# Kernel optimization log

Measured on AMD Instinct MI355X. Metric: run time of the kernel, lower is better.

Reference implementation:

```python
import jax, jax.numpy as jnp
import numpy as np


def lstm_cell(x, h, c, Wi, Wh, b):
    # PyTorch LSTMCell gate order: i, f, g, o
    g = x @ Wi.T + h @ Wh.T + b
    i, f, gg, o = jnp.split(g, 4, axis=-1)
    c = jax.nn.sigmoid(f) * c + jax.nn.sigmoid(i) * jnp.tanh(gg)
    h = jax.nn.sigmoid(o) * jnp.tanh(c)
    return h, c


def setup_inputs() -> dict:
    key = jax.random.key(0)
    ks = jax.random.split(key, 32)
    S, B, L, N, T = 20, 16, 30, 6, 20
    H, E, Vs, Vt = 512, 512, 50000, 30000
    w = lambda k, shape: jax.random.normal(k, shape, jnp.float32) * 0.05
    return {
        'articles': jax.random.randint(ks[0], (S, B, L), 0, Vs, jnp.int32),
        'summaries': jax.random.randint(ks[1], (N, B, T), 0, Vt, jnp.int32),
        'emb_src': w(ks[2], (Vs, E)),
        'emb_tgt': w(ks[3], (Vt, E)),
        'we_Wi': w(ks[4], (4 * H, E)), 'we_Wh': w(ks[5], (4 * H, H)), 'we_b': w(ks[6], (4 * H,)),
        'se_Wi': w(ks[7], (4 * H, H)), 'se_Wh': w(ks[8], (4 * H, H)), 'se_b': w(ks[9], (4 * H,)),
        'W_feat': w(ks[10], (H, H)), 'b_feat': w(ks[11], (H,)),
        'wd_Wi': w(ks[12], (4 * H, E)), 'wd_Wh': w(ks[13], (4 * H, H)), 'wd_b': w(ks[14], (4 * H,)),
        'W_vocab': w(ks[15], (Vt, H)), 'b_vocab': w(ks[16], (Vt,)),
        'sd_Wi': w(ks[17], (4 * H, H)), 'sd_Wh': w(ks[18], (4 * H, H)), 'sd_b': w(ks[19], (4 * H,)),
        'attn_Wh': w(ks[20], (H, H)), 'attn_wc': w(ks[21], (H,)), 'attn_v': w(ks[22], (H,)),
        'W_out': w(ks[23], (H, 2 * H)), 'b_out': w(ks[24], (H,)),
    }


def _forward(articles, summaries, emb_src, emb_tgt, we_Wi, we_Wh, we_b,
             se_Wi, se_Wh, se_b, W_feat, b_feat, wd_Wi, wd_Wh, wd_b,
             W_vocab, b_vocab, sd_Wi, sd_Wh, sd_b, attn_Wh, attn_wc, attn_v,
             W_out, b_out):
    S, B, L = articles.shape
    H = we_Wh.shape[1]

    # ---- word encoder: LSTMCell over each sentence, vmapped over S ----
    def encode_sentence(tokens):  # [B, L]
        x = emb_src[tokens]  # [B, L, E]
        z = jnp.zeros((B, H), x.dtype)
        def step(hc, xt):
            h, c = lstm_cell(xt, hc[0], hc[1], we_Wi, we_Wh, we_b)
            return (h, c), None
        (h, _), _ = jax.lax.scan(step, (z, z), jnp.swapaxes(x, 0, 1))
        return h
    word_hx = jax.vmap(encode_sentence)(articles)  # [S, B, H]

    # ---- sentence encoder: LSTM over sentence dim ----
    z = jnp.zeros((B, H), word_hx.dtype)
    def senc_step(hc, x):
        h, c = lstm_cell(x, hc[0], hc[1], se_Wi, se_Wh, se_b)
        return (h, c), h
    (s_hx, s_cx), sent_out = jax.lax.scan(senc_step, (z, z), word_hx)  # sent_out [S,B,H]
    sent_feat = sent_out @ W_feat.T + b_feat  # precomputed attention features

    mask = (articles[:, :, 0:1] > 0).astype(jnp.float32)  # [S, B, 1]
    coverage0 = jnp.zeros_like(mask)

    # ---- hierarchical decoder over summary sentences ----
    def sent_step(carry, sent):  # sent [B, T]
        w_hx, w_cx, s_hx, s_cx, coverage, loss = carry
        seq = sent.T  # [T, B]

        def word_step(wc, ba):
            wh, wcell, l = wc
            wb, wa = ba
            wh, wcell = lstm_cell(emb_tgt[wb], wh, wcell, wd_Wi, wd_Wh, wd_b)
            logits = wh @ W_vocab.T + b_vocab  # [B, V]
            logp = jax.nn.log_softmax(logits, axis=-1)
            nll = -jnp.take_along_axis(logp, wa[:, None], axis=1)[:, 0]
            m = (wa != 0).astype(logits.dtype)  # ignore_index=0
            l = l + jnp.sum(nll * m) / jnp.maximum(jnp.sum(m), 1.0)
            return (wh, wcell, l), None

        (w_hx, w_cx, loss), _ = jax.lax.scan(word_step, (w_hx, w_cx, loss), (seq[:-1], seq[1:]))

        # sentence decoder step with coverage attention over S sentences
        s_h2, s_cx = lstm_cell(w_hx, s_hx, s_cx, sd_Wi, sd_Wh, sd_b)
        e = jnp.einsum('sbh,h->sb', jnp.tanh(sent_feat + s_h2 @ attn_Wh.T + coverage * attn_wc), attn_v)
        e = jnp.where(mask[:, :, 0] > 0, e, -1e9)
        align = jax.nn.softmax(e, axis=0)[:, :, None]  # [S, B, 1]
        context = jnp.sum(align * sent_out, axis=0)  # [B, H]
        final = jnp.tanh(jnp.concatenate([context, s_h2], axis=-1) @ W_out.T + b_out)
        # coverage loss (with pre-update coverage), then accumulate coverage
        loss = loss + jnp.mean(jnp.sum(jnp.minimum(align[:, :, 0], coverage[:, :, 0]), axis=0))
        coverage = coverage + align
        return (final, w_cx, final, s_cx, coverage, loss), None

    init = (s_hx, s_cx, s_hx, s_cx, coverage0, jnp.float32(0.0))
    (_, _, _, _, _, loss), _ = jax.lax.scan(sent_step, init, summaries)
    return loss


def reference(articles, summaries, emb_src, emb_tgt, we_Wi, we_Wh, we_b,
              se_Wi, se_Wh, se_b, W_feat, b_feat, wd_Wi, wd_Wh, wd_b,
              W_vocab, b_vocab, sd_Wi, sd_Wh, sd_b, attn_Wh, attn_wc, attn_v,
              W_out, b_out):
    return _forward(articles, summaries, emb_src, emb_tgt, we_Wi, we_Wh, we_b,
                    se_Wi, se_Wh, se_b, W_feat, b_feat, wd_Wi, wd_Wh, wd_b,
                    W_vocab, b_vocab, sd_Wi, sd_Wh, sd_b, attn_Wh, attn_wc,
                    attn_v, W_out, b_out)
```

## Files before the change

### kernel.cpp

```cpp
#include <hip/hip_runtime.h>
#include <cstdint>
#include <cstddef>

#define H 512
#define SS 20
#define BB 16
#define LL 30
#define NN 6
#define TT 20
#define VT 30000
#define MROWS 1824
#define NSTEPS 114
#define MPAD 1856
#define NT2 120
#define UBLK 16
#define NV 232
#define MEGA 248

#define SCOPE_AGENT __HIP_MEMORY_SCOPE_AGENT

typedef __attribute__((ext_vector_type(8))) short bf16x8;
typedef __attribute__((ext_vector_type(4))) float f32x4;

__device__ __forceinline__ float sigmoidf_(float x) { return 1.f / (1.f + expf(-x)); }
__device__ __forceinline__ float b2f(ushort u) { return __uint_as_float(((uint32_t)u) << 16); }
__device__ __forceinline__ ushort f2b_rne(float f) {
  uint32_t u = __float_as_uint(f);
  return (ushort)((u + 0x7fffu + ((u >> 16) & 1u)) >> 16);
}

__device__ __forceinline__ void ast_u32(uint* p, uint v) {
  __hip_atomic_store(p, v, __ATOMIC_RELAXED, SCOPE_AGENT);
}
__device__ __forceinline__ uint ald_u32(const uint* p) {
  return __hip_atomic_load(p, __ATOMIC_RELAXED, SCOPE_AGENT);
}

__device__ __forceinline__ void sbar(uint* flags, int slot, int nblk, uint phase)
{
  __syncthreads();
  if (threadIdx.x == 0) {
    __builtin_amdgcn_fence(__ATOMIC_RELEASE, "agent");
    ast_u32(&flags[slot * 16], phase);
  }
  if ((int)threadIdx.x < nblk) {
    while (ald_u32(&flags[threadIdx.x * 16]) < phase)
      __builtin_amdgcn_s_sleep(1);
  }
  __syncthreads();
  if (threadIdx.x == 0)
    __builtin_amdgcn_fence(__ATOMIC_ACQUIRE, "agent");
  __syncthreads();
}

struct PrepP {
  const int* articles; const int* summaries;
  const float* emb_src; const float* emb_tgt;
  const float* we_Wi; const float* wd_Wi; const float* we_Wh;
  const float* se_Wi; const float* se_Wh; const float* W_feat;
  const float* wd_Wh; const float* sd_Wi; const float* sd_Wh;
  const float* attn_Wh; const float* W_out;
  ushort* A_we; ushort* A_wd;
  ushort* weWi; ushort* wdWi; ushort* weWh;
  ushort* seWi; ushort* seWh; ushort* wfeat;
  ushort* wdWh; ushort* sdWi; ushort* sdWh;
  ushort* attnWh; ushort* Wout;
};

__device__ __forceinline__ void conv_f2b(const float* __restrict__ src,
                                         ushort* __restrict__ dst, int n4,
                                         int t0, int stride)
{
  for (int i = t0; i < n4; i += stride) {
    float4 v = reinterpret_cast<const float4*>(src)[i];
    ushort4 o;
    o.x = f2b_rne(v.x); o.y = f2b_rne(v.y);
    o.z = f2b_rne(v.z); o.w = f2b_rne(v.w);
    reinterpret_cast<ushort4*>(dst)[i] = o;
  }
}

__global__ __launch_bounds__(256) void prep_kernel(PrepP P)
{
  const int t0 = blockIdx.x * 256 + threadIdx.x;
  const int stride = gridDim.x * 256;
  for (int i = t0; i < SS * BB * LL * H; i += stride) {
    int m = i >> 9, k = i & 511;
    int l = m / (SS * BB), sb = m % (SS * BB);
    int tok = P.articles[sb * LL + l];
    P.A_we[i] = f2b_rne(P.emb_src[(size_t)tok * H + k]);
  }
  for (int i = t0; i < MROWS * H; i += stride) {
    int m = i >> 9, k = i & 511;
    int stp = m >> 4, b = m & 15;
    int n = stp / (TT - 1), t = stp % (TT - 1);
    int tok = P.summaries[(n * BB + b) * TT + t];
    P.A_wd[i] = f2b_rne(P.emb_tgt[(size_t)tok * H + k]);
  }
  const int Q = 4 * H * H / 4;
  conv_f2b(P.we_Wi, P.weWi, Q, t0, stride);
  conv_f2b(P.wd_Wi, P.wdWi, Q, t0, stride);
  conv_f2b(P.we_Wh, P.weWh, Q, t0, stride);
  conv_f2b(P.se_Wi, P.seWi, Q, t0, stride);
  conv_f2b(P.se_Wh, P.seWh, Q, t0, stride);
  conv_f2b(P.wd_Wh, P.wdWh, Q, t0, stride);
  conv_f2b(P.sd_Wi, P.sdWi, Q, t0, stride);
  conv_f2b(P.sd_Wh, P.sdWh, Q, t0, stride);
  conv_f2b(P.W_feat, P.wfeat, H * H / 4, t0, stride);
  conv_f2b(P.attn_Wh, P.attnWh, H * H / 4, t0, stride);
  conv_f2b(P.W_out, P.Wout, H * 2 * H / 4, t0, stride);
}

__global__ __launch_bounds__(512) void proj_mfma_kernel(
    const ushort* __restrict__ A_we, const ushort* __restrict__ weWi,
    const float* __restrict__ we_b, ushort* __restrict__ XiW,
    const ushort* __restrict__ A_wd, const ushort* __restrict__ wdWi,
    const float* __restrict__ wd_b, ushort* __restrict__ XiD)
{
  int bid = blockIdx.x;
  const ushort* A; const ushort* W; const float* bias; ushort* C; int M, mt, nt;
  if (bid < 1200) { A = A_we; W = weWi; bias = we_b; C = XiW; M = 9600; mt = bid >> 3; nt = bid & 7; }
  else { int b2 = bid - 1200; A = A_wd; W = wdWi; bias = wd_b; C = XiD; M = MROWS; mt = b2 >> 3; nt = b2 & 7; }
  const int tid = threadIdx.x, wid = tid >> 6, lane = tid & 63;
  const int wm = wid >> 2, wn = wid & 3;
  const int m0 = mt * 64 + wm * 32, n0 = nt * 256 + wn * 64;
  const int lr = lane & 15, lk = (lane >> 4) << 3;

  f32x4 acc[2][4];
#pragma unroll
  for (int i = 0; i < 2; ++i)
#pragma unroll
    for (int nf = 0; nf < 4; ++nf) acc[i][nf] = (f32x4)0.0f;

  for (int k0 = 0; k0 < H; k0 += 32) {
    bf16x8 a[2], b[4];
#pragma unroll
    for (int i = 0; i < 2; ++i) {
      int m = m0 + i * 16 + lr;
      bf16x8 az = (bf16x8)(short)0;
      if (m < M) az = *reinterpret_cast<const bf16x8*>(A + (size_t)m * H + k0 + lk);
      a[i] = az;
    }
#pragma unroll
    for (int nf = 0; nf < 4; ++nf)
      b[nf] = *reinterpret_cast<const bf16x8*>(W + (size_t)(n0 + nf * 16 + lr) * H + k0 + lk);
#pragma unroll
    for (int i = 0; i < 2; ++i)
#pragma unroll
      for (int nf = 0; nf < 4; ++nf)
        acc[i][nf] = __builtin_amdgcn_mfma_f32_16x16x32_bf16(a[i], b[nf], acc[i][nf], 0, 0, 0);
  }
#pragma unroll
  for (int i = 0; i < 2; ++i)
#pragma unroll
    for (int nf = 0; nf < 4; ++nf) {
      int n = n0 + nf * 16 + lr;
      float bv = bias[n];
#pragma unroll
      for (int jreg = 0; jreg < 4; ++jreg) {
        int row = m0 + i * 16 + (lane >> 4) * 4 + jreg;
        if (row < M) C[(size_t)row * 2048 + n] = f2b_rne(acc[i][nf][jreg] + bv);
      }
    }
}

struct MP {
  const ushort* XiW; const ushort* XiD;
  const ushort* weWh; const ushort* seWi; const ushort* seWh;
  const ushort* wfeat; const ushort* wdWh; const ushort* sdWi;
  const ushort* sdWh; const ushort* attnWh; const ushort* Wout;
  const float* se_b; const float* b_feat; const float* sd_b; const float* b_out;
  const float* attn_wc; const float* attn_v; const int* articles;
  ushort* h0; ushort* h1;
  float* XiS;
  ushort* sh0; ushort* sh1;
  float* sent_out; ushort* sent_out_bf; float* sent_feat;
  ushort* wh_bf; ushort* sdh_bf; ushort* final_bf; ushort* catb;
  float* qb; float* ebuf; float* alignb; float* covb; float* loss;
  uint* sflags;
  uint* vbflags;
  uint* vflag;
  const float* Wv; ushort* Wv_bf; const float* bv; float* partials;
};

__global__ __launch_bounds__(512) void mega_kernel(MP P)
{
  const int tid = threadIdx.x, bid = blockIdx.x;
  const int wid = tid >> 6, lane = tid & 63;
  const int lr = lane & 15;
  const int lk = (lane >> 4) << 3;
  const int orow = (lane >> 4) << 2;

  if (bid >= UBLK) {
    const int v = bid - UBLK;
    const int mt = v >> 3, chunk = v & 7;
    __shared__ float red[4][64][2];

    if (tid == 0) {
      while (ald_u32(P.vflag) < 1u) __builtin_amdgcn_s_sleep(16);
    }
    __syncthreads();
    {
      const int n4 = VT * H / 4;
      for (int i = v * 512 + tid; i < n4; i += NV * 512) {
        float4 w = reinterpret_cast<const float4*>(P.Wv)[i];
        ushort4 o;
        o.x = f2b_rne(w.x); o.y = f2b_rne(w.y);
        o.z = f2b_rne(w.z); o.w = f2b_rne(w.w);
        reinterpret_cast<ushort4*>(P.Wv_bf)[i] = o;
      }
    }
    sbar(P.vbflags, v, NV, 1u);

    {
      int lastStep = mt * 4 + 3; if (lastStep > 113) lastStep = 113;
      uint want = 2u + (uint)(lastStep / 19);
      if (tid == 0) {
        while (ald_u32(P.vflag) < want) __builtin_amdgcn_s_sleep(16);
        __builtin_amdgcn_fence(__ATOMIC_ACQUIRE, "agent");
      }
      __syncthreads();
    }

    const int wm = wid >> 2, wn = wid & 3;
    const int m0 = mt * 64 + wm * 32;
    bf16x8 areg[2][16];
#pragma unroll
    for (int i = 0; i < 2; ++i)
#pragma unroll
      for (int kk = 0; kk < 16; ++kk)
        areg[i][kk] = *reinterpret_cast<const bf16x8*>(
            P.wh_bf + (size_t)(m0 + i * 16 + lr) * H + kk * 32 + lk);

    for (int nt2 = 0; nt2 < 15; ++nt2) {
      const int n0 = chunk * 3840 + nt2 * 256 + wn * 64;
      f32x4 acc[2][4];
#pragma unroll
      for (int i = 0; i < 2; ++i)
#pragma unroll
        for (int nf = 0; nf < 4; ++nf) acc[i][nf] = (f32x4)0.0f;

#pragma unroll 4
      for (int kk = 0; kk < 16; ++kk) {
        bf16x8 b[4];
#pragma unroll
        for (int nf = 0; nf < 4; ++nf) {
          int n = n0 + nf * 16 + lr;
          bf16x8 bz = (bf16x8)(short)0;
          if (n < VT) bz = *reinterpret_cast<const bf16x8*>(P.Wv_bf + (size_t)n * H + kk * 32 + lk);
          b[nf] = bz;
        }
#pragma unroll
        for (int i = 0; i < 2; ++i)
#pragma unroll
          for (int nf = 0; nf < 4; ++nf)
            acc[i][nf] = __builtin_amdgcn_mfma_f32_16x16x32_bf16(areg[i][kk], b[nf], acc[i][nf], 0, 0, 0);
      }

      float bc[4];
      int val[4];
#pragma unroll
      for (int nf = 0; nf < 4; ++nf) {
        int n = n0 + nf * 16 + lr;
        val[nf] = (n < VT);
        bc[nf] = val[nf] ? P.bv[n] : 0.f;
      }
#pragma unroll
      for (int i = 0; i < 2; ++i) {
#pragma unroll
        for (int jreg = 0; jreg < 4; ++jreg) {
          float lg[4];
          float mx = -3.0e38f;
#pragma unroll
          for (int nf = 0; nf < 4; ++nf) {
            lg[nf] = val[nf] ? (acc[i][nf][jreg] + bc[nf]) : -3.0e38f;
            mx = fmaxf(mx, lg[nf]);
          }
#pragma unroll
          for (int d = 1; d < 16; d <<= 1) mx = fmaxf(mx, __shfl_xor(mx, d));
          float s = 0.f;
#pragma unroll
          for (int nf = 0; nf < 4; ++nf) s += val[nf] ? expf(lg[nf] - mx) : 0.f;
#pragma unroll
          for (int d = 1; d < 16; d <<= 1) s += __shfl_xor(s, d);
          if (lr == 0) {
            int rloc = wm * 32 + i * 16 + (lane >> 4) * 4 + jreg;
            red[wn][rloc][0] = mx;
            red[wn][rloc][1] = s;
          }
        }
      }
      __syncthreads();
      if (tid < 64) {
        int r2 = tid;
        float M = -3.0e38f;
#pragma unroll
        for (int w = 0; w < 4; ++w) M = fmaxf(M, red[w][r2][0]);
        float S = 0.f;
#pragma unroll
        for (int w = 0; w < 4; ++w) S += red[w][r2][1] * expf(red[w][r2][0] - M);
        size_t p = ((size_t)(mt * 64 + r2) * NT2 + chunk * 15 + nt2) * 2;
        P.partials[p] = M;
        P.partials[p + 1] = S;
      }
      __syncthreads();
    }
    return;
  }

  __shared__ f32x4 hred[2][4][64];
  const int gw = bid * 8 + wid;
  uint ph = 0;

  {
    float cst[5][4];
#pragma unroll
    for (int it = 0; it < 5; ++it)
#pragma unroll
      for (int rg = 0; rg < 4; ++rg) cst[it][rg] = 0.f;
    ushort* cur = P.h0;
    ushort* nxt = P.h1;
    const int ug = gw & 31;
    const int unit = ug * 16 + lr;
    const ushort* wb = P.weWh + (size_t)(ug * 16 + lr) * H + lk;
    for (int l = 0; l < LL; ++l) {
#pragma unroll
      for (int it = 0; it < 5; ++it) {
        int mt = (gw + it * 128) >> 5;
        f32x4 acc[4];
#pragma unroll
        for (int g = 0; g < 4; ++g) acc[g] = (f32x4)0.0f;
        const ushort* ab = cur + (size_t)(mt * 16 + lr) * H + lk;
#pragma unroll
        for (int k0 = 0; k0 < H; k0 += 32) {
          bf16x8 a = *reinterpret_cast<const bf16x8*>(ab + k0);
#pragma unroll
          for (int g = 0; g < 4; ++g) {
            bf16x8 b = *reinterpret_cast<const bf16x8*>(wb + (size_t)g * H * H + k0);
            acc[g] = __builtin_amdgcn_mfma_f32_16x16x32_bf16(a, b, acc[g], 0, 0, 0);
          }
        }
#pragma unroll
        for (int rg = 0; rg < 4; ++rg) {
          int row = mt * 16 + orow + rg;
          const ushort* xi = P.XiW + (size_t)(l * 320 + row) * 2048 + unit;
          float gi = acc[0][rg] + b2f(xi[0]);
          float gf = acc[1][rg] + b2f(xi[512]);
          float gc = acc[2][rg] + b2f(xi[1024]);
          float go = acc[3][rg] + b2f(xi[1536]);
          float c = sigmoidf_(gf) * cst[it][rg] + sigmoidf_(gi) * tanhf(gc);
          float h = sigmoidf_(go) * tanhf(c);
          cst[it][rg] = c;
          nxt[(size_t)row * H + unit] = f2b_rne(h);
        }
      }
      sbar(P.sflags, bid, UBLK, ++ph);
      ushort* t = cur; cur = nxt; nxt = t;
    }
    {
      const ushort* wbs = P.seWi + (size_t)(ug * 16 + lr) * H + lk;
#pragma unroll
      for (int it = 0; it < 5; ++it) {
        int mt = (gw + it * 128) >> 5;
        f32x4 acc[4];
#pragma unroll
        for (int g = 0; g < 4; ++g) acc[g] = (f32x4)0.0f;
        const ushort* ab = cur + (size_t)(mt * 16 + lr) * H + lk;
#pragma unroll
        for (int k0 = 0; k0 < H; k0 += 32) {
          bf16x8 a = *reinterpret_cast<const bf16x8*>(ab + k0);
#pragma unroll
          for (int g = 0; g < 4; ++g) {
            bf16x8 b = *reinterpret_cast<const bf16x8*>(wbs + (size_t)g * H * H + k0);
            acc[g] = __builtin_amdgcn_mfma_f32_16x16x32_bf16(a, b, acc[g], 0, 0, 0);
          }
        }
#pragma unroll
        for (int rg = 0; rg < 4; ++rg) {
          int row = mt * 16 + orow + rg;
#pragma unroll
          for (int g = 0; g < 4; ++g)
            P.XiS[(size_t)row * 2048 + g * H + unit] = acc[g][rg] + P.se_b[g * H + unit];
        }
      }
    }
    sbar(P.sflags, bid, UBLK, ++ph);
    if (bid == 0 && tid == 0)
      __hip_atomic_store(P.vflag, 1u, __ATOMIC_RELEASE, SCOPE_AGENT);
  }

  float cw[4] = {0.f, 0.f, 0.f, 0.f};
  float csd[4] = {0.f, 0.f, 0.f, 0.f};
  {
    float cse[4] = {0.f, 0.f, 0.f, 0.f};
    ushort* cur = P.sh0;
    ushort* nxt = P.sh1;
    const int ug = bid * 2 + wid;
    const int unit = ug * 16 + lr;
    for (int s = 0; s < SS; ++s) {
      if (wid < 2) {
        f32x4 acc[4];
#pragma unroll
        for (int g = 0; g < 4; ++g) acc[g] = (f32x4)0.0f;
        const ushort* ab = cur + (size_t)lr * H + lk;
        const ushort* wb = P.seWh + (size_t)(ug * 16 + lr) * H + lk;
#pragma unroll
        for (int k0 = 0; k0 < H; k0 += 32) {
          bf16x8 a = *reinterpret_cast<const bf16x8*>(ab + k0);
#pragma unroll
          for (int g = 0; g < 4; ++g) {
            bf16x8 b = *reinterpret_cast<const bf16x8*>(wb + (size_t)g * H * H + k0);
            acc[g] = __builtin_amdgcn_mfma_f32_16x16x32_bf16(a, b, acc[g], 0, 0, 0);
          }
        }
#pragma unroll
        for (int rg = 0; rg < 4; ++rg) {
          int row = orow + rg;
          const float* xi = P.XiS + (size_t)(s * 16 + row) * 2048 + unit;
          float gi = acc[0][rg] + xi[0];
          float gf = acc[1][rg] + xi[512];
          float gc = acc[2][rg] + xi[1024];
          float go = acc[3][rg] + xi[1536];
          float c = sigmoidf_(gf) * cse[rg] + sigmoidf_(gi) * tanhf(gc);
          float h = sigmoidf_(go) * tanhf(c);
          cse[rg] = c;
          nxt[(size_t)row * H + unit] = f2b_rne(h);
          P.sent_out[(size_t)(s * 16 + row) * H + unit] = h;
          P.sent_out_bf[(size_t)(s * 16 + row) * H + unit] = f2b_rne(h);
        }
      }
      sbar(P.sflags, bid, UBLK, ++ph);
      ushort* t = cur; cur = nxt; nxt = t;
    }
    if (wid < 2) {
      f32x4 v; v[0] = cse[0]; v[1] = cse[1]; v[2] = cse[2]; v[3] = cse[3];
      hred[wid][0][lane] = v;
#pragma unroll
      for (int rg = 0; rg < 4; ++rg) csd[rg] = cse[rg];
    }
    __syncthreads();
    if (wid < 4 && !(wid & 1)) {
      f32x4 v = hred[wid >> 1][0][lane];
      cw[0] = v[0]; cw[1] = v[1]; cw[2] = v[2]; cw[3] = v[3];
    }
    __syncthreads();
  }

  {
    const int ug = gw & 31;
    const int unit = ug * 16 + lr;
    const ushort* wb = P.wfeat + (size_t)(ug * 16 + lr) * H + lk;
#pragma unroll
    for (int it = 0; it < 5; ++it) {
      int mt = (gw + it * 128) >> 5;
      f32x4 acc = (f32x4)0.0f;
      const ushort* ab = P.sent_out_bf + (size_t)(mt * 16 + lr) * H + lk;
#pragma unroll
      for (int k0 = 0; k0 < H; k0 += 32) {
        bf16x8 a = *reinterpret_cast<const bf16x8*>(ab + k0);
        bf16x8 b = *reinterpret_cast<const bf16x8*>(wb + k0);
        acc = __builtin_amdgcn_mfma_f32_16x16x32_bf16(a, b, acc, 0, 0, 0);
      }
#pragma unroll
      for (int rg = 0; rg < 4; ++rg) {
        int row = mt * 16 + orow + rg;
        P.sent_feat[(size_t)row * H + unit] = acc[rg] + P.b_feat[unit];
      }
    }
    sbar(P.sflags, bid, UBLK, ++ph);
  }

  {
    const int half = wid & 1;
    const int ug2 = bid * 2 + (wid >> 1);
    const int unit2 = ug2 * 16 + lr;
    const int ug = bid * 2 + wid;
    const int unit = ug * 16 + lr;

    for (int n = 0; n < NN; ++n) {
      bf16x8 wreg[4][8];
      if (wid < 4) {
#pragma unroll
        for (int g = 0; g < 4; ++g)
#pragma unroll
          for (int kk = 0; kk < 8; ++kk)
            wreg[g][kk] = *reinterpret_cast<const bf16x8*>(
                P.wdWh + (size_t)g * H * H + (size_t)(ug2 * 16 + lr) * H +
                half * 256 + kk * 32 + lk);
      }
      for (int t = 0; t < TT - 1; ++t) {
        int stp = n * (TT - 1) + t;
        f32x4 acc[4];
        if (wid < 4) {
          const ushort* A = (t == 0)
              ? ((n == 0) ? P.sh0 : P.final_bf)
              : P.wh_bf + (size_t)(stp - 1) * 16 * H;
#pragma unroll
          for (int g = 0; g < 4; ++g) acc[g] = (f32x4)0.0f;
          const ushort* ab = A + (size_t)lr * H + half * 256 + lk;
#pragma unroll
          for (int kk = 0; kk < 8; ++kk) {
            bf16x8 a = *reinterpret_cast<const bf16x8*>(ab + kk * 32);
#pragma unroll
            for (int g = 0; g < 4; ++g)
              acc[g] = __builtin_amdgcn_mfma_f32_16x16x32_bf16(a, wreg[g][kk], acc[g], 0, 0, 0);
          }
          if (half) {
#pragma unroll
            for (int g = 0; g < 4; ++g) hred[wid >> 1][g][lane] = acc[g];
          }
        }
        __syncthreads();
        if (wid < 4 && !half) {
#pragma unroll
          for (int g = 0; g < 4; ++g) acc[g] += hred[wid >> 1][g][lane];
#pragma unroll
          for (int rg = 0; rg < 4; ++rg) {
            int row = orow + rg;
            const ushort* xi = P.XiD + (size_t)(stp * 16 + row) * 2048 + unit2;
            float gi = acc[0][rg] + b2f(xi[0]);
            float gf = acc[1][rg] + b2f(xi[512]);
            float gc = acc[2][rg] + b2f(xi[1024]);
            float go = acc[3][rg] + b2f(xi[1536]);
            float c = sigmoidf_(gf) * cw[rg] + sigmoidf_(gi) * tanhf(gc);
            float h = sigmoidf_(go) * tanhf(c);
            cw[rg] = c;
            P.wh_bf[(size_t)(stp * 16 + row) * H + unit2] = f2b_rne(h);
          }
        }
        sbar(P.sflags, bid, UBLK, ++ph);
      }
      if (bid == 0 && tid == 0)
        __hip_atomic_store(P.vflag, 2u + (uint)n, __ATOMIC_RELEASE, SCOPE_AGENT);
      if (wid < 2) {
        f32x4 acc[4];
#pragma unroll
        for (int g = 0; g < 4; ++g) acc[g] = (f32x4)0.0f;
        const ushort* A1 = P.wh_bf + (size_t)(n * (TT - 1) + TT - 2) * 16 * H;
        const ushort* A2 = (n == 0) ? P.sh0 : P.final_bf;
        const ushort* ab1 = A1 + (size_t)lr * H + lk;
        const ushort* wb1 = P.sdWi + (size_t)(ug * 16 + lr) * H + lk;
#pragma unroll
        for (int k0 = 0; k0 < H; k0 += 32) {
          bf16x8 a = *reinterpret_cast<const bf16x8*>(ab1 + k0);
#pragma unroll
          for (int g = 0; g < 4; ++g) {
            bf16x8 b = *reinterpret_cast<const bf16x8*>(wb1 + (size_t)g * H * H + k0);
            acc[g] = __builtin_amdgcn_mfma_f32_16x16x32_bf16(a, b, acc[g], 0, 0, 0);
          }
        }
        const ushort* ab2 = A2 + (size_t)lr * H + lk;
        const ushort* wb2 = P.sdWh + (size_t)(ug * 16 + lr) * H + lk;
#pragma unroll
        for (int k0 = 0; k0 < H; k0 += 32) {
          bf16x8 a = *reinterpret_cast<const bf16x8*>(ab2 + k0);
#pragma unroll
          for (int g = 0; g < 4; ++g) {
            bf16x8 b = *reinterpret_cast<const bf16x8*>(wb2 + (size_t)g * H * H + k0);
            acc[g] = __builtin_amdgcn_mfma_f32_16x16x32_bf16(a, b, acc[g], 0, 0, 0);
          }
        }
#pragma unroll
        for (int rg = 0; rg < 4; ++rg) {
          int row = orow + rg;
          float gi = acc[0][rg] + P.sd_b[0 * H + unit];
          float gf = acc[1][rg] + P.sd_b[1 * H + unit];
          float gc = acc[2][rg] + P.sd_b[2 * H + unit];
          float go = acc[3][rg] + P.sd_b[3 * H + unit];
          float c = sigmoidf_(gf) * csd[rg] + sigmoidf_(gi) * tanhf(gc);
          float h = sigmoidf_(go) * tanhf(c);
          csd[rg] = c;
          P.sdh_bf[(size_t)row * H + unit] = f2b_rne(h);
        }
      }
      sbar(P.sflags, bid, UBLK, ++ph);
      if (wid < 2) {
        f32x4 acc = (f32x4)0.0f;
        const ushort* ab = P.sdh_bf + (size_t)lr * H + lk;
        const ushort* wb = P.attnWh + (size_t)(ug * 16 + lr) * H + lk;
#pragma unroll
        for (int k0 = 0; k0 < H; k0 += 32) {
          bf16x8 a = *reinterpret_cast<const bf16x8*>(ab + k0);
          bf16x8 b = *reinterpret_cast<const bf16x8*>(wb + k0);
          acc = __builtin_amdgcn_mfma_f32_16x16x32_bf16(a, b, acc, 0, 0, 0);
        }
#pragma unroll
        for (int rg = 0; rg < 4; ++rg)
          P.qb[(size_t)(orow + rg) * H + unit] = acc[rg];
      }
      sbar(P.sflags, bid, UBLK, ++ph);
      for (int sb = gw; sb < 320; sb += 128) {
        int b = sb & 15;
        float cov = P.covb[sb];
        float sum = 0.f;
        for (int h2 = lane; h2 < H; h2 += 64)
          sum += tanhf(P.sent_feat[(size_t)sb * H + h2] + P.qb[b * H + h2] +
                       cov * P.attn_wc[h2]) * P.attn_v[h2];
#pragma unroll
        for (int d = 1; d < 64; d <<= 1) sum += __shfl_xor(sum, d);
        if (lane == 0)
          P.ebuf[sb] = (P.articles[sb * LL] > 0) ? sum : -1e9f;
      }
      sbar(P.sflags, bid, UBLK, ++ph);
      if (wid == 0) {
        int b = bid;
        float ev = (lane < SS) ? P.ebuf[lane * 16 + b] : -3.0e38f;
        float mx = ev;
#pragma unroll
        for (int d = 1; d < 64; d <<= 1) mx = fmaxf(mx, __shfl_xor(mx, d));
        float ex = (lane < SS) ? expf(ev - mx) : 0.f;
        float s = ex;
#pragma unroll
        for (int d = 1; d < 64; d <<= 1) s += __shfl_xor(s, d);
        float al = ex / s;
        float cl = 0.f;
        if (lane < SS) {
          int sb = lane * 16 + b;
          float cov = P.covb[sb];
          cl = fminf(al, cov);
          P.covb[sb] = cov + al;
          P.alignb[sb] = al;
        }
#pragma unroll
        for (int d = 1; d < 64; d <<= 1) cl += __shfl_xor(cl, d);
        if (lane == 0) atomicAdd(P.loss, cl * (1.f / BB));
      }
      __syncthreads();
      {
        int b = bid, h2 = tid;
        float s = 0.f;
#pragma unroll
        for (int ss2 = 0; ss2 < SS; ++ss2)
          s += P.alignb[ss2 * 16 + b] * P.sent_out[(size_t)(ss2 * 16 + b) * H + h2];
        P.catb[b * 1024 + h2] = f2b_rne(s);
        P.catb[b * 1024 + 512 + h2] = P.sdh_bf[(size_t)b * H + h2];
      }
      sbar(P.sflags, bid, UBLK, ++ph);
      if (wid < 2) {
        f32x4 acc = (f32x4)0.0f;
        const ushort* ab = P.catb + (size_t)lr * 1024 + lk;
        const ushort* wb = P.Wout + (size_t)(ug * 16 + lr) * 1024 + lk;
#pragma unroll
        for (int k0 = 0; k0 < 1024; k0 += 32) {
          bf16x8 a = *reinterpret_cast<const bf16x8*>(ab + k0);
          bf16x8 b = *reinterpret_cast<const bf16x8*>(wb + k0);
          acc = __builtin_amdgcn_mfma_f32_16x16x32_bf16(a, b, acc, 0, 0, 0);
        }
#pragma unroll
        for (int rg = 0; rg < 4; ++rg) {
          int row = orow + rg;
          float v = tanhf(acc[rg] + P.b_out[unit]);
          P.final_bf[(size_t)row * H + unit] = f2b_rne(v);
        }
      }
      sbar(P.sflags, bid, UBLK, ++ph);
    }
    if (bid == 0 && tid == 0)
      __hip_atomic_store(P.vflag, 7u, __ATOMIC_RELEASE, SCOPE_AGENT);
  }
}

__global__ void tlog_kernel(const ushort* __restrict__ wh_bf,
                            const ushort* __restrict__ Wv_bf,
                            const float* __restrict__ bv,
                            const int* __restrict__ summaries,
                            float* __restrict__ tlog)
{
  int row = blockIdx.x;
  int lane = threadIdx.x;
  int b = row & 15, stp = row >> 4;
  int n = stp / (TT - 1), t = stp % (TT - 1);
  int tgt = summaries[(n * BB + b) * TT + t + 1];
  float s = 0.f;
  for (int k = lane; k < H; k += 64)
    s += b2f(wh_bf[(size_t)row * H + k]) * b2f(Wv_bf[(size_t)tgt * H + k]);
#pragma unroll
  for (int d = 1; d < 64; d <<= 1) s += __shfl_xor(s, d);
  if (lane == 0) tlog[row] = s + bv[tgt];
}

__global__ __launch_bounds__(256) void nll_kernel(
    const float* __restrict__ partials, const float* __restrict__ tlog,
    const int* __restrict__ summaries, float* __restrict__ loss)
{
  int stp = blockIdx.x;
  int tid = threadIdx.x;
  int rr = tid >> 4, ch = tid & 15;
  int row = stp * 16 + rr;
  const float* pr = partials + (size_t)row * NT2 * 2;
  float mx = -3.0e38f;
  for (int t2 = ch; t2 < NT2; t2 += 16) mx = fmaxf(mx, pr[t2 * 2]);
#pragma unroll
  for (int d = 1; d < 16; d <<= 1) mx = fmaxf(mx, __shfl_xor(mx, d));
  float s = 0.f;
  for (int t2 = ch; t2 < NT2; t2 += 16) s += pr[t2 * 2 + 1] * expf(pr[t2 * 2] - mx);
#pragma unroll
  for (int d = 1; d < 16; d <<= 1) s += __shfl_xor(s, d);
  __shared__ float sh_n[16], sh_m[16];
  if (ch == 0) {
    float lse = mx + logf(s);
    float nll = lse - tlog[row];
    int b = row & 15;
    int n = stp / (TT - 1), t = stp % (TT - 1);
    int wa = summaries[(n * BB + b) * TT + t + 1];
    sh_n[rr] = (wa != 0) ? nll : 0.f;
    sh_m[rr] = (wa != 0) ? 1.f : 0.f;
  }
  __syncthreads();
  if (tid == 0) {
    float sn = 0.f, sm = 0.f;
    for (int r2 = 0; r2 < 16; ++r2) { sn += sh_n[r2]; sm += sh_m[r2]; }
    atomicAdd(loss, sn / fmaxf(sm, 1.f));
  }
}

extern "C" void kernel_launch(void* const* d_in, const int* in_sizes, int n_in,
                              void* d_out, int out_size, void* d_ws, size_t ws_size,
                              hipStream_t stream)
{
  (void)in_sizes; (void)n_in; (void)out_size; (void)ws_size;
  const int*   articles  = (const int*)d_in[0];
  const int*   summaries = (const int*)d_in[1];
  const float* emb_src   = (const float*)d_in[2];
  const float* emb_tgt   = (const float*)d_in[3];
  const float* we_Wi = (const float*)d_in[4];
  const float* we_Wh = (const float*)d_in[5];
  const float* we_b  = (const float*)d_in[6];
  const float* se_Wi = (const float*)d_in[7];
  const float* se_Wh = (const float*)d_in[8];
  const float* se_b  = (const float*)d_in[9];
  const float* W_feat = (const float*)d_in[10];
  const float* b_feat = (const float*)d_in[11];
  const float* wd_Wi = (const float*)d_in[12];
  const float* wd_Wh = (const float*)d_in[13];
  const float* wd_b  = (const float*)d_in[14];
  const float* W_vocab = (const float*)d_in[15];
  const float* b_vocab = (const float*)d_in[16];
  const float* sd_Wi = (const float*)d_in[17];
  const float* sd_Wh = (const float*)d_in[18];
  const float* sd_b  = (const float*)d_in[19];
  const float* attn_Wh = (const float*)d_in[20];
  const float* attn_wc = (const float*)d_in[21];
  const float* attn_v  = (const float*)d_in[22];
  const float* W_out = (const float*)d_in[23];
  const float* b_out = (const float*)d_in[24];

  char* wsb = (char*)d_ws;
  size_t off = 0;
  auto alloc = [&](size_t bytes) -> char* {
    char* p = wsb + off;
    off += (bytes + 255) & ~(size_t)255;
    return p;
  };

  char* regA = alloc(9830400);
  ushort* A_we     = (ushort*)regA;
  ushort* wh_bf    = (ushort*)regA;
  float*  partials = (float*)(regA + 1900544);
  float*  tlogb    = (float*)(regA + 3682304);

  ushort* A_wd = (ushort*)alloc((size_t)MROWS * H * 2);

  char* regW = alloc((size_t)9600 * 2048 * 2);
  ushort* XiW   = (ushort*)regW;
  ushort* Wv_bf = (ushort*)regW;

  ushort* XiD = (ushort*)alloc((size_t)MROWS * 2048 * 2);

  ushort* weWi  = (ushort*)alloc(4 * H * H * 2);
  ushort* wdWi  = (ushort*)alloc(4 * H * H * 2);
  ushort* weWh  = (ushort*)alloc(4 * H * H * 2);
  ushort* seWi  = (ushort*)alloc(4 * H * H * 2);
  ushort* seWh  = (ushort*)alloc(4 * H * H * 2);
  ushort* wdWh  = (ushort*)alloc(4 * H * H * 2);
  ushort* sdWi  = (ushort*)alloc(4 * H * H * 2);
  ushort* sdWh  = (ushort*)alloc(4 * H * H * 2);
  ushort* wfeat = (ushort*)alloc(H * H * 2);
  ushort* attnWh= (ushort*)alloc(H * H * 2);
  ushort* Wout  = (ushort*)alloc(H * 2 * H * 2);

  float*  XiS = (float*)alloc((size_t)320 * 2048 * 4);
  ushort* h0  = (ushort*)alloc(320 * H * 2);
  ushort* h1  = (ushort*)alloc(320 * H * 2);
  ushort* sh0 = (ushort*)alloc(16 * H * 2);
  ushort* sh1 = (ushort*)alloc(16 * H * 2);
  float*  sent_out    = (float*)alloc(320 * H * 4);
  ushort* sent_out_bf = (ushort*)alloc(320 * H * 2);
  float*  sent_feat   = (float*)alloc(320 * H * 4);
  ushort* sdh_bf   = (ushort*)alloc(16 * H * 2);
  ushort* final_bf = (ushort*)alloc(16 * H * 2);
  ushort* catb     = (ushort*)alloc(16 * 1024 * 2);
  float*  qb       = (float*)alloc(16 * H * 4);
  float*  ebuf   = (float*)alloc(1280);
  float*  alignb = (float*)alloc(1280);
  float*  covb   = (float*)alloc(1280);
  uint*   sflags  = (uint*)alloc(UBLK * 16 * 4);
  uint*   vbflags = (uint*)alloc(NV * 16 * 4);
  uint*   vflag   = (uint*)alloc(256);

  float* loss = (float*)d_out;
  hipMemsetAsync(loss, 0, 4, stream);
  hipMemsetAsync(covb, 0, 1280, stream);
  hipMemsetAsync(h0, 0, 320 * H * 2, stream);
  hipMemsetAsync(sh0, 0, 16 * H * 2, stream);
  hipMemsetAsync(sflags, 0, UBLK * 16 * 4, stream);
  hipMemsetAsync(vbflags, 0, NV * 16 * 4, stream);
  hipMemsetAsync(vflag, 0, 256, stream);

  {
    PrepP P = {articles, summaries, emb_src, emb_tgt,
               we_Wi, wd_Wi, we_Wh, se_Wi, se_Wh, W_feat,
               wd_Wh, sd_Wi, sd_Wh, attn_Wh, W_out,
               A_we, A_wd, weWi, wdWi, weWh, seWi, seWh, wfeat,
               wdWh, sdWi, sdWh, attnWh, Wout};
    prep_kernel<<<2048, 256, 0, stream>>>(P);
  }

  proj_mfma_kernel<<<1432, 512, 0, stream>>>(A_we, weWi, we_b, XiW,
                                             A_wd, wdWi, wd_b, XiD);

  hipMemsetAsync((char*)wh_bf + (size_t)MROWS * H * 2, 0,
                 (size_t)(MPAD - MROWS) * H * 2, stream);

  {
    MP P;
    P.XiW = XiW; P.XiD = XiD;
    P.weWh = weWh; P.seWi = seWi; P.seWh = seWh; P.wfeat = wfeat;
    P.wdWh = wdWh; P.sdWi = sdWi; P.sdWh = sdWh; P.attnWh = attnWh; P.Wout = Wout;
    P.se_b = se_b; P.b_feat = b_feat; P.sd_b = sd_b; P.b_out = b_out;
    P.attn_wc = attn_wc; P.attn_v = attn_v; P.articles = articles;
    P.h0 = h0; P.h1 = h1; P.XiS = XiS; P.sh0 = sh0; P.sh1 = sh1;
    P.sent_out = sent_out; P.sent_out_bf = sent_out_bf; P.sent_feat = sent_feat;
    P.wh_bf = wh_bf; P.sdh_bf = sdh_bf; P.final_bf = final_bf; P.catb = catb;
    P.qb = qb; P.ebuf = ebuf; P.alignb = alignb; P.covb = covb; P.loss = loss;
    P.sflags = sflags; P.vbflags = vbflags; P.vflag = vflag;
    P.Wv = W_vocab; P.Wv_bf = Wv_bf; P.bv = b_vocab; P.partials = partials;
    mega_kernel<<<MEGA, 512, 0, stream>>>(P);
  }

  tlog_kernel<<<MROWS, 64, 0, stream>>>(wh_bf, Wv_bf, b_vocab, summaries, tlogb);
  nll_kernel<<<NSTEPS, 256, 0, stream>>>(partials, tlogb, summaries, loss);
}
```

Before: 5.032 ms.

## Spread sequential blocks across XCDs and keep attention state per block in LDS

The 16 sequential recurrence blocks now use block ids that are multiples of 8 below 128, so they land on different XCDs instead of packing onto one. The vocab-worker blocks are renumbered to fill the remaining ids. Each sequential block owns one batch element, so the attention energies, alignment and coverage now live in shared memory. This drops one grid-wide barrier per decoder step along with the global ebuf, alignb and covb buffers. The risks are more L2 traffic across XCDs for shared recurrent state, and each block now computes all 20 energies for its batch element, which adds some per-block work.

```diff
diff --git a/kernel.cpp b/kernel.cpp
--- a/kernel.cpp
+++ b/kernel.cpp
@@ -176,7 +176,7 @@
   ushort* sh0; ushort* sh1;
   float* sent_out; ushort* sent_out_bf; float* sent_feat;
   ushort* wh_bf; ushort* sdh_bf; ushort* final_bf; ushort* catb;
-  float* qb; float* ebuf; float* alignb; float* covb; float* loss;
+  float* qb; float* loss;
   uint* sflags;
   uint* vbflags;
   uint* vflag;
@@ -191,8 +191,10 @@
   const int lk = (lane >> 4) << 3;
   const int orow = (lane >> 4) << 2;
 
-  if (bid >= UBLK) {
-    const int v = bid - UBLK;
+  const bool isSeq = (bid < 128) && ((bid & 7) == 0);
+
+  if (!isSeq) {
+    const int v = (bid < 128) ? (bid - (bid >> 3) - 1) : (bid - UBLK);
     const int mt = v >> 3, chunk = v & 7;
     __shared__ float red[4][64][2];
 
@@ -213,8 +215,8 @@
     sbar(P.vbflags, v, NV, 1u);
 
     {
-      int lastStep = mt * 4 + 3; if (lastStep > 113) lastStep = 113;
-      uint want = 2u + (uint)(lastStep / 19);
+      int lastStep = mt * 4 + 3; if (lastStep > NSTEPS - 1) lastStep = NSTEPS - 1;
+      uint want = 2u + (uint)(lastStep / (TT - 1));
       if (tid == 0) {
         while (ald_u32(P.vflag) < want) __builtin_amdgcn_s_sleep(16);
         __builtin_amdgcn_fence(__ATOMIC_ACQUIRE, "agent");
@@ -295,10 +297,10 @@
         int r2 = tid;
         float M = -3.0e38f;
 #pragma unroll
-        for (int w = 0; w < 4; ++w) M = fmaxf(M, red[w][r2][0]);
+        for (int q = 0; q < 4; ++q) M = fmaxf(M, red[q][r2][0]);
         float S = 0.f;
 #pragma unroll
-        for (int w = 0; w < 4; ++w) S += red[w][r2][1] * expf(red[w][r2][0] - M);
+        for (int q = 0; q < 4; ++q) S += red[q][r2][1] * expf(red[q][r2][0] - M);
         size_t p = ((size_t)(mt * 64 + r2) * NT2 + chunk * 15 + nt2) * 2;
         P.partials[p] = M;
         P.partials[p + 1] = S;
@@ -308,8 +310,10 @@
     return;
   }
 
+  const int sid = bid >> 3;
   __shared__ f32x4 hred[2][4][64];
-  const int gw = bid * 8 + wid;
+  __shared__ float e_l[SS], align_l[SS], cov_l[SS];
+  const int gw = sid * 8 + wid;
   uint ph = 0;
 
   {
@@ -354,7 +358,7 @@
           nxt[(size_t)row * H + unit] = f2b_rne(h);
         }
       }
-      sbar(P.sflags, bid, UBLK, ++ph);
+      sbar(P.sflags, sid, UBLK, ++ph);
       ushort* t = cur; cur = nxt; nxt = t;
     }
     {
@@ -384,8 +388,8 @@
         }
       }
     }
-    sbar(P.sflags, bid, UBLK, ++ph);
-    if (bid == 0 && tid == 0)
+    sbar(P.sflags, sid, UBLK, ++ph);
+    if (sid == 0 && tid == 0)
       __hip_atomic_store(P.vflag, 1u, __ATOMIC_RELEASE, SCOPE_AGENT);
   }
 
@@ -395,7 +399,7 @@
     float cse[4] = {0.f, 0.f, 0.f, 0.f};
     ushort* cur = P.sh0;
     ushort* nxt = P.sh1;
-    const int ug = bid * 2 + wid;
+    const int ug = sid * 2 + wid;
     const int unit = ug * 16 + lr;
     for (int s = 0; s < SS; ++s) {
       if (wid < 2) {
@@ -429,7 +433,7 @@
           P.sent_out_bf[(size_t)(s * 16 + row) * H + unit] = f2b_rne(h);
         }
       }
-      sbar(P.sflags, bid, UBLK, ++ph);
+      sbar(P.sflags, sid, UBLK, ++ph);
       ushort* t = cur; cur = nxt; nxt = t;
     }
     if (wid < 2) {
@@ -467,15 +471,17 @@
         P.sent_feat[(size_t)row * H + unit] = acc[rg] + P.b_feat[unit];
       }
     }
-    sbar(P.sflags, bid, UBLK, ++ph);
+    if (tid < SS) cov_l[tid] = 0.f;
+    sbar(P.sflags, sid, UBLK, ++ph);
   }
 
   {
     const int half = wid & 1;
-    const int ug2 = bid * 2 + (wid >> 1);
+    const int ug2 = sid * 2 + (wid >> 1);
     const int unit2 = ug2 * 16 + lr;
-    const int ug = bid * 2 + wid;
+    const int ug = sid * 2 + wid;
     const int unit = ug * 16 + lr;
+    const int b_ = sid;
 
     for (int n = 0; n < NN; ++n) {
       bf16x8 wreg[4][8];
@@ -528,9 +534,9 @@
             P.wh_bf[(size_t)(stp * 16 + row) * H + unit2] = f2b_rne(h);
           }
         }
-        sbar(P.sflags, bid, UBLK, ++ph);
-      }
-      if (bid == 0 && tid == 0)
+        sbar(P.sflags, sid, UBLK, ++ph);
+      }
+      if (sid == 0 && tid == 0)
         __hip_atomic_store(P.vflag, 2u + (uint)n, __ATOMIC_RELEASE, SCOPE_AGENT);
       if (wid < 2) {
         f32x4 acc[4];
@@ -573,7 +579,7 @@
           P.sdh_bf[(size_t)row * H + unit] = f2b_rne(h);
         }
       }
-      sbar(P.sflags, bid, UBLK, ++ph);
+      sbar(P.sflags, sid, UBLK, ++ph);
       if (wid < 2) {
         f32x4 acc = (f32x4)0.0f;
         const ushort* ab = P.sdh_bf + (size_t)lr * H + lk;
@@ -588,23 +594,21 @@
         for (int rg = 0; rg < 4; ++rg)
           P.qb[(size_t)(orow + rg) * H + unit] = acc[rg];
       }
-      sbar(P.sflags, bid, UBLK, ++ph);
-      for (int sb = gw; sb < 320; sb += 128) {
-        int b = sb & 15;
-        float cov = P.covb[sb];
+      sbar(P.sflags, sid, UBLK, ++ph);
+      for (int s = wid; s < SS; s += 8) {
+        float cov = cov_l[s];
         float sum = 0.f;
         for (int h2 = lane; h2 < H; h2 += 64)
-          sum += tanhf(P.sent_feat[(size_t)sb * H + h2] + P.qb[b * H + h2] +
-                       cov * P.attn_wc[h2]) * P.attn_v[h2];
+          sum += tanhf(P.sent_feat[(size_t)(s * 16 + b_) * H + h2] +
+                       P.qb[b_ * H + h2] + cov * P.attn_wc[h2]) * P.attn_v[h2];
 #pragma unroll
         for (int d = 1; d < 64; d <<= 1) sum += __shfl_xor(sum, d);
         if (lane == 0)
-          P.ebuf[sb] = (P.articles[sb * LL] > 0) ? sum : -1e9f;
-      }
-      sbar(P.sflags, bid, UBLK, ++ph);
+          e_l[s] = (P.articles[(s * 16 + b_) * LL] > 0) ? sum : -1e9f;
+      }
+      __syncthreads();
       if (wid == 0) {
-        int b = bid;
-        float ev = (lane < SS) ? P.ebuf[lane * 16 + b] : -3.0e38f;
+        float ev = (lane < SS) ? e_l[lane] : -3.0e38f;
         float mx = ev;
 #pragma unroll
         for (int d = 1; d < 64; d <<= 1) mx = fmaxf(mx, __shfl_xor(mx, d));
@@ -615,27 +619,25 @@
         float al = ex / s;
         float cl = 0.f;
         if (lane < SS) {
-          int sb = lane * 16 + b;
-          float cov = P.covb[sb];
+          float cov = cov_l[lane];
           cl = fminf(al, cov);
-          P.covb[sb] = cov + al;
-          P.alignb[sb] = al;
+          cov_l[lane] = cov + al;
+          align_l[lane] = al;
         }
 #pragma unroll
         for (int d = 1; d < 64; d <<= 1) cl += __shfl_xor(cl, d);
         if (lane == 0) atomicAdd(P.loss, cl * (1.f / BB));
       }
       __syncthreads();
-      {
-        int b = bid, h2 = tid;
+      if (tid < 512) {
         float s = 0.f;
 #pragma unroll
         for (int ss2 = 0; ss2 < SS; ++ss2)
-          s += P.alignb[ss2 * 16 + b] * P.sent_out[(size_t)(ss2 * 16 + b) * H + h2];
-        P.catb[b * 1024 + h2] = f2b_rne(s);
-        P.catb[b * 1024 + 512 + h2] = P.sdh_bf[(size_t)b * H + h2];
-      }
-      sbar(P.sflags, bid, UBLK, ++ph);
+          s += align_l[ss2] * P.sent_out[(size_t)(ss2 * 16 + b_) * H + tid];
+        P.catb[b_ * 1024 + tid] = f2b_rne(s);
+        P.catb[b_ * 1024 + 512 + tid] = P.sdh_bf[(size_t)b_ * H + tid];
+      }
+      sbar(P.sflags, sid, UBLK, ++ph);
       if (wid < 2) {
         f32x4 acc = (f32x4)0.0f;
         const ushort* ab = P.catb + (size_t)lr * 1024 + lk;
@@ -653,9 +655,9 @@
           P.final_bf[(size_t)row * H + unit] = f2b_rne(v);
         }
       }
-      sbar(P.sflags, bid, UBLK, ++ph);
-    }
-    if (bid == 0 && tid == 0)
+      sbar(P.sflags, sid, UBLK, ++ph);
+    }
+    if (sid == 0 && tid == 0)
       __hip_atomic_store(P.vflag, 7u, __ATOMIC_RELEASE, SCOPE_AGENT);
   }
 }
@@ -791,16 +793,12 @@
   ushort* final_bf = (ushort*)alloc(16 * H * 2);
   ushort* catb     = (ushort*)alloc(16 * 1024 * 2);
   float*  qb       = (float*)alloc(16 * H * 4);
-  float*  ebuf   = (float*)alloc(1280);
-  float*  alignb = (float*)alloc(1280);
-  float*  covb   = (float*)alloc(1280);
   uint*   sflags  = (uint*)alloc(UBLK * 16 * 4);
   uint*   vbflags = (uint*)alloc(NV * 16 * 4);
   uint*   vflag   = (uint*)alloc(256);
 
   float* loss = (float*)d_out;
   hipMemsetAsync(loss, 0, 4, stream);
-  hipMemsetAsync(covb, 0, 1280, stream);
   hipMemsetAsync(h0, 0, 320 * H * 2, stream);
   hipMemsetAsync(sh0, 0, 16 * H * 2, stream);
   hipMemsetAsync(sflags, 0, UBLK * 16 * 4, stream);
@@ -832,7 +830,7 @@
     P.h0 = h0; P.h1 = h1; P.XiS = XiS; P.sh0 = sh0; P.sh1 = sh1;
     P.sent_out = sent_out; P.sent_out_bf = sent_out_bf; P.sent_feat = sent_feat;
     P.wh_bf = wh_bf; P.sdh_bf = sdh_bf; P.final_bf = final_bf; P.catb = catb;
-    P.qb = qb; P.ebuf = ebuf; P.alignb = alignb; P.covb = covb; P.loss = loss;
+    P.qb = qb; P.loss = loss;
     P.sflags = sflags; P.vbflags = vbflags; P.vflag = vflag;
     P.Wv = W_vocab; P.Wv_bf = Wv_bf; P.bv = b_vocab; P.partials = partials;
     mega_kernel<<<MEGA, 512, 0, stream>>>(P);
```

Result: slower. 5.429 ms (+7.9%).
